# Kernel tuning notes

Hardware: AMD Instinct MI355X
Metric: run time of the kernel (lower is better)

The kernel has to match this reference:

```python
import jax, jax.numpy as jnp
import numpy as np

DIM = 1024
WIN = 7
HEADS = 16
HEAD_DIM = DIM // HEADS
NT = WIN * WIN  # tokens per window = 49


def _relative_position_index():
    coords = np.stack(np.meshgrid(np.arange(WIN), np.arange(WIN), indexing='ij'))  # [2,W,W]
    cf = coords.reshape(2, -1)  # [2, NT]
    rel = cf[:, :, None] - cf[:, None, :]  # [2, NT, NT]
    rel = rel.transpose(1, 2, 0).copy()
    rel[:, :, 0] += WIN - 1
    rel[:, :, 1] += WIN - 1
    rel[:, :, 0] *= 2 * WIN - 1
    return jnp.asarray(rel.sum(-1), dtype=jnp.int32)  # [NT, NT]

REL_IDX = _relative_position_index()


def setup_inputs() -> dict:
    key = jax.random.key(0)
    ks = jax.random.split(key, 7)
    bsz_windows = 2048
    num_windows = 64
    x = jax.random.normal(ks[0], (bsz_windows, NT, DIM), dtype=jnp.float32)
    attn_mask = jax.random.normal(ks[1], (num_windows, NT, NT), dtype=jnp.float32)
    s = 0.02
    qkv_w = jax.random.normal(ks[2], (3 * DIM, DIM), dtype=jnp.float32) * s
    qkv_b = jnp.zeros((3 * DIM,), dtype=jnp.float32)
    proj_w = jax.random.normal(ks[3], (DIM, DIM), dtype=jnp.float32) * s
    proj_b = jnp.zeros((DIM,), dtype=jnp.float32)
    bias_table = jax.random.normal(ks[4], ((2 * WIN - 1) ** 2, HEADS), dtype=jnp.float32) * s
    return {"x": x, "attn_mask": attn_mask, "qkv_w": qkv_w, "qkv_b": qkv_b,
            "proj_w": proj_w, "proj_b": proj_b, "bias_table": bias_table}


def reference(x, attn_mask, qkv_w, qkv_b, proj_w, proj_b, bias_table):
    bw, nt, c = x.shape
    scale = HEAD_DIM ** -0.5
    qkv = x @ qkv_w.T + qkv_b  # [bw, nt, 3*dim]
    qkv = qkv.reshape(bw, nt, 3, HEADS, HEAD_DIM).transpose(2, 0, 3, 1, 4)
    q, k, v = qkv[0], qkv[1], qkv[2]  # each [bw, h, nt, hd]
    attn = jnp.einsum('bhqd,bhkd->bhqk', q * scale, k)  # [bw, h, nt, nt]
    rel_bias = bias_table[REL_IDX.reshape(-1)].reshape(nt, nt, HEADS).transpose(2, 0, 1)
    attn = attn + rel_bias[None]
    nw = attn_mask.shape[0]
    attn = attn.reshape(bw // nw, nw, HEADS, nt, nt) + attn_mask[None, :, None]
    attn = attn.reshape(bw, HEADS, nt, nt)
    attn = jax.nn.softmax(attn, axis=-1)
    out = jnp.einsum('bhqk,bhkd->bhqd', attn, v)
    out = out.transpose(0, 2, 1, 3).reshape(bw, nt, c)
    return out @ proj_w.T + proj_b
```

## Files before the change

kernel.cpp:

```cpp
#include <hip/hip_runtime.h>
#include <hip/hip_bf16.h>
#include <cstdint>
#include <cstddef>

#define HEADS 16
#define HD 64
#define NT 49
#define NTOK 3136
#define MROWS 100352
#define KDIM 1024

typedef __attribute__((ext_vector_type(4))) float f32x4;
typedef __attribute__((ext_vector_type(8))) short bf16x8;
typedef __attribute__((ext_vector_type(4))) unsigned short u16x4;

__device__ __forceinline__ unsigned short f2b(float f) {
  __hip_bfloat16 h = __float2bfloat16(f);
  return *reinterpret_cast<unsigned short*>(&h);
}
__device__ __forceinline__ float b2f(unsigned short u) {
  union { unsigned int i; float f; } c; c.i = ((unsigned int)u) << 16; return c.f;
}

__device__ __forceinline__ void gload16(const unsigned short* g, void* l) {
  __builtin_amdgcn_global_load_lds(
      (const __attribute__((address_space(1))) void*)g,
      (__attribute__((address_space(3))) void*)l, 16, 0, 0);
}

__device__ __forceinline__ void bar() {
  asm volatile("" ::: "memory");
  __builtin_amdgcn_s_barrier();
  asm volatile("" ::: "memory");
}

__global__ void cvt_f32_bf16(const float* __restrict__ s,
                             unsigned short* __restrict__ d, long n4) {
  long stride = (long)gridDim.x * blockDim.x;
  for (long i = blockIdx.x * (long)blockDim.x + threadIdx.x; i < n4; i += stride) {
    f32x4 v = reinterpret_cast<const f32x4*>(s)[i];
    u16x4 o;
    o.x = f2b(v.x); o.y = f2b(v.y); o.z = f2b(v.z); o.w = f2b(v.w);
    reinterpret_cast<u16x4*>(d)[i] = o;
  }
}

__global__ void build_bm(const float* __restrict__ mask,
                         const float* __restrict__ bias_table,
                         float* __restrict__ bm) {
  const int wm = blockIdx.x >> 4, h = blockIdx.x & 15;
  const float* mrow = mask + (size_t)wm * (NT * NT);
  float* dst = bm + ((size_t)wm * HEADS + h) * (NT * 64);
  for (int idx = threadIdx.x; idx < NT * 64; idx += 256) {
    const int a = idx >> 6, b = idx & 63;
    float v = -1e30f;
    if (b < NT) {
      const int ia = a / 7, ja = a - ia * 7;
      const int ib = b / 7, jb = b - ib * 7;
      v = mrow[a * NT + b] +
          bias_table[((ia - ib + 6) * 13 + (ja - jb + 6)) * HEADS + h];
    }
    dst[idx] = v;
  }
}

template<int EPI>
__global__ __launch_bounds__(512, 2)
void gemm_bt(const unsigned short* __restrict__ A,
             const unsigned short* __restrict__ B,
             const float* __restrict__ bias,
             void* __restrict__ Cout,
             const int nTilesN) {
  __shared__ __align__(16) unsigned short lds[2 * 2 * 256 * 64];

  const int nwg = gridDim.x;
  const int bid = blockIdx.x;
  const int cpx = nwg >> 3;
  const int swz = (bid & 7) * cpx + (bid >> 3);
  const int mt = swz / nTilesN;
  const int nt = swz - mt * nTilesN;
  const long mBase = (long)mt * 256;
  const int nBase = nt * 256;

  const int tid = threadIdx.x;
  const int lane = tid & 63;
  const int wid = tid >> 6;
  const int wr = wid >> 2;
  const int wc = wid & 3;
  const int lr = lane & 15;
  const int kg = lane >> 4;

  const int rbase = tid >> 3;
  const int c8 = (((tid & 7) ^ (rbase & 7)) << 3);
  const unsigned short* aSrc = A + (size_t)(mBase + rbase) * KDIM + c8;
  const unsigned short* bSrc = B + (size_t)(nBase + rbase) * KDIM + c8;
  char* ldsB = (char*)lds;

  f32x4 acc[8][4] = {};

  const int aRow = (wr * 128 + lr) * 64;
  const int bRow = (wc * 64 + lr) * 64;
  const int fOff0 = ((0 * 4 + kg) ^ (lr & 7)) << 3;
  const int fOff1 = ((1 * 4 + kg) ^ (lr & 7)) << 3;

#define STAGE(buf, kt) do {                                         \
    char* dA = ldsB + (buf) * 65536 + tid * 16;                     \
    const unsigned short* sA = aSrc + (kt) * 64;                    \
    const unsigned short* sB = bSrc + (kt) * 64;                    \
    _Pragma("unroll")                                               \
    for (int j = 0; j < 4; ++j)                                     \
      gload16(sA + (size_t)j * 64 * KDIM, dA + j * 8192);           \
    _Pragma("unroll")                                               \
    for (int j = 0; j < 4; ++j)                                     \
      gload16(sB + (size_t)j * 64 * KDIM, dA + 32768 + j * 8192);   \
  } while (0)

  STAGE(0, 0);
  STAGE(1, 1);
  asm volatile("s_waitcnt vmcnt(8)" ::: "memory");
  __builtin_amdgcn_sched_barrier(0);
  bar();

  for (int kt = 0; kt < KDIM / 64; ++kt) {
    const int cb = kt & 1;
    const unsigned short* As = lds + cb * 32768;
    const unsigned short* Bs = As + 16384;

    bf16x8 a0[4], a1[4], a2[4], a3[4], b0[4], b1[4];

#pragma unroll
    for (int j = 0; j < 4; ++j)
      a0[j] = *reinterpret_cast<const bf16x8*>(As + aRow + j * 1024 + fOff0);
#pragma unroll
    for (int n = 0; n < 4; ++n)
      b0[n] = *reinterpret_cast<const bf16x8*>(Bs + bRow + n * 1024 + fOff0);

    __builtin_amdgcn_s_setprio(1);
#pragma unroll
    for (int j = 0; j < 4; ++j)
      a1[j] = *reinterpret_cast<const bf16x8*>(As + aRow + (4 + j) * 1024 + fOff0);
#pragma unroll
    for (int j = 0; j < 4; ++j)
#pragma unroll
      for (int n = 0; n < 4; ++n)
        acc[j][n] = __builtin_amdgcn_mfma_f32_16x16x32_bf16(
            a0[j], b0[n], acc[j][n], 0, 0, 0);
    __builtin_amdgcn_s_setprio(0);
    bar();

    __builtin_amdgcn_s_setprio(1);
#pragma unroll
    for (int j = 0; j < 4; ++j)
      a2[j] = *reinterpret_cast<const bf16x8*>(As + aRow + j * 1024 + fOff1);
#pragma unroll
    for (int n = 0; n < 4; ++n)
      b1[n] = *reinterpret_cast<const bf16x8*>(Bs + bRow + n * 1024 + fOff1);
#pragma unroll
    for (int j = 0; j < 4; ++j)
#pragma unroll
      for (int n = 0; n < 4; ++n)
        acc[4 + j][n] = __builtin_amdgcn_mfma_f32_16x16x32_bf16(
            a1[j], b0[n], acc[4 + j][n], 0, 0, 0);
    __builtin_amdgcn_s_setprio(0);
    bar();

    __builtin_amdgcn_s_setprio(1);
#pragma unroll
    for (int j = 0; j < 4; ++j)
      a3[j] = *reinterpret_cast<const bf16x8*>(As + aRow + (4 + j) * 1024 + fOff1);
#pragma unroll
    for (int j = 0; j < 4; ++j)
#pragma unroll
      for (int n = 0; n < 4; ++n)
        acc[j][n] = __builtin_amdgcn_mfma_f32_16x16x32_bf16(
            a2[j], b1[n], acc[j][n], 0, 0, 0);
    __builtin_amdgcn_s_setprio(0);
    bar();

    __builtin_amdgcn_s_setprio(1);
#pragma unroll
    for (int j = 0; j < 4; ++j)
#pragma unroll
      for (int n = 0; n < 4; ++n)
        acc[4 + j][n] = __builtin_amdgcn_mfma_f32_16x16x32_bf16(
            a3[j], b1[n], acc[4 + j][n], 0, 0, 0);
    __builtin_amdgcn_s_setprio(0);
    bar();

    if (kt < KDIM / 64 - 2) {
      STAGE(cb, kt + 2);
      asm volatile("s_waitcnt vmcnt(8)" ::: "memory");
      __builtin_amdgcn_sched_barrier(0);
      bar();
    } else if (kt == KDIM / 64 - 2) {
      asm volatile("s_waitcnt vmcnt(0)" ::: "memory");
      __builtin_amdgcn_sched_barrier(0);
      bar();
    }
  }
#undef STAGE

  if (EPI == 0) {
    unsigned short* qkvbuf = (unsigned short*)Cout;
#pragma unroll
    for (int m = 0; m < 8; ++m) {
      const int row0 = wr * 128 + m * 16 + kg * 4;
#pragma unroll
      for (int n = 0; n < 4; ++n) {
        const int col = nBase + wc * 64 + n * 16 + lr;
        const int which = col >> 10;
        const int head = (col >> 6) & 15;
        const int d = col & 63;
        const float bv = bias[col];
#pragma unroll
        for (int r = 0; r < 4; ++r) {
          const int gm = (int)mBase + row0 + r;
          const int w = gm / NT;
          const int t = gm - w * NT;
          float v = acc[m][n][r] + bv;
          if (which == 0) v *= 0.125f;
          qkvbuf[(((size_t)w * 3 + which) * HEADS + head) * NTOK + t * HD + d] =
              f2b(v);
        }
      }
    }
  } else {
    float* out = (float*)Cout;
#pragma unroll
    for (int m = 0; m < 8; ++m) {
      const int row0 = wr * 128 + m * 16 + kg * 4;
#pragma unroll
      for (int n = 0; n < 4; ++n) {
        const int col = nBase + wc * 64 + n * 16 + lr;
        const float bv = bias[col];
#pragma unroll
        for (int r = 0; r < 4; ++r) {
          const int gm = (int)mBase + row0 + r;
          out[(size_t)gm * KDIM + col] = acc[m][n][r] + bv;
        }
      }
    }
  }
}

#define PSTR 72
#define VTSTR 72

__global__ __launch_bounds__(256, 8)
void attn_mfma(const unsigned short* __restrict__ qkv,
               const float* __restrict__ bm,
               unsigned short* __restrict__ aout) {
  const int blk = blockIdx.x;
  const int w = blk >> 4;
  const int h = blk & 15;
  const int tid = threadIdx.x;
  const int lane = tid & 63;
  const int wv = tid >> 6;
  const int lr = lane & 15;
  const int kg = lane >> 4;

  __shared__ __align__(16) unsigned short Plds[64 * PSTR];
  __shared__ __align__(16) unsigned short VldsT[64 * VTSTR];

  const unsigned short* qp = qkv + (((size_t)w * 3 + 0) * HEADS + h) * NTOK;
  const unsigned short* kp = qp + (size_t)HEADS * NTOK;
  const unsigned short* vp = qp + (size_t)2 * HEADS * NTOK;
  const float* bmrow = bm + (((size_t)(w & 63) * HEADS + h) * (NT * 64));

  const int a0 = wv * 16 + kg * 4;
  f32x4 acc[4];
#pragma unroll
  for (int r = 0; r < 4; ++r) {
    const int a = a0 + r;
    const int ar = (a > 48) ? 48 : a;
#pragma unroll
    for (int n = 0; n < 4; ++n)
      acc[n][r] = bmrow[ar * 64 + n * 16 + lr];
  }

#pragma unroll
  for (int i = 0; i < 4; ++i) {
    const int idx = i * 256 + tid;
    if (idx < 784) {
      const int t = idx >> 4, c4 = (idx & 15) * 4;
      u16x4 vv = *reinterpret_cast<const u16x4*>(vp + t * HD + c4);
      const int ts = t >> 3, t7 = t & 7;
#pragma unroll
      for (int ii = 0; ii < 4; ++ii) {
        const int d = c4 + ii;
        VldsT[d * VTSTR + (((ts ^ (d & 7)) << 3) + t7)] =
            ((const unsigned short*)&vv)[ii];
      }
    }
  }
#pragma unroll
  for (int i = 0; i < 4; ++i) {
    const int idx = i * 256 + tid;
    if (idx < 960) {
      const int d = idx / 15, t = 49 + idx - d * 15;
      VldsT[d * VTSTR + ((((t >> 3) ^ (d & 7)) << 3) + (t & 7))] = 0;
    }
  }
  __syncthreads();

  int qrow = wv * 16 + lr; if (qrow > 48) qrow = 48;
#pragma unroll
  for (int ks = 0; ks < 2; ++ks) {
    bf16x8 af = *reinterpret_cast<const bf16x8*>(qp + qrow * HD + ks * 32 + kg * 8);
#pragma unroll
    for (int n = 0; n < 4; ++n) {
      int row = n * 16 + lr; if (row > 48) row = 48;
      bf16x8 bfr = *reinterpret_cast<const bf16x8*>(kp + row * HD + ks * 32 + kg * 8);
      acc[n] = __builtin_amdgcn_mfma_f32_16x16x32_bf16(af, bfr, acc[n], 0, 0, 0);
    }
  }

#pragma unroll
  for (int r = 0; r < 4; ++r) {
    float mx = fmaxf(fmaxf(acc[0][r], acc[1][r]),
                     fmaxf(acc[2][r], acc[3][r]));
    mx = fmaxf(mx, __shfl_xor(mx, 1));
    mx = fmaxf(mx, __shfl_xor(mx, 2));
    mx = fmaxf(mx, __shfl_xor(mx, 4));
    mx = fmaxf(mx, __shfl_xor(mx, 8));
    float s = 0.f;
#pragma unroll
    for (int n = 0; n < 4; ++n) {
      const float e = __expf(acc[n][r] - mx);
      acc[n][r] = e;
      s += e;
    }
    s += __shfl_xor(s, 1);
    s += __shfl_xor(s, 2);
    s += __shfl_xor(s, 4);
    s += __shfl_xor(s, 8);
    const float si = 1.0f / s;
#pragma unroll
    for (int n = 0; n < 4; ++n) acc[n][r] *= si;
  }

#pragma unroll
  for (int n = 0; n < 4; ++n)
#pragma unroll
    for (int r = 0; r < 4; ++r)
      Plds[(a0 + r) * PSTR + n * 16 + lr] = f2b(acc[n][r]);

  f32x4 acc2[4] = {};
  const int prow = wv * 16 + lr;
#pragma unroll
  for (int ks = 0; ks < 2; ++ks) {
    bf16x8 pf = *reinterpret_cast<const bf16x8*>(
        &Plds[prow * PSTR + ks * 32 + kg * 8]);
#pragma unroll
    for (int n = 0; n < 4; ++n) {
      const int d = n * 16 + lr;
      bf16x8 vf = *reinterpret_cast<const bf16x8*>(
          &VldsT[d * VTSTR + ((((ks * 4 + kg) ^ (d & 7)) << 3))]);
      acc2[n] = __builtin_amdgcn_mfma_f32_16x16x32_bf16(pf, vf, acc2[n], 0, 0, 0);
    }
  }

#pragma unroll
  for (int r = 0; r < 4; ++r) {
    const int a = a0 + r;
    if (a >= NT) continue;
#pragma unroll
    for (int n = 0; n < 4; ++n) {
      const int d = n * 16 + lr;
      aout[((size_t)(w * NT + a)) * KDIM + h * HD + d] = f2b(acc2[n][r]);
    }
  }
}

extern "C" void kernel_launch(void* const* d_in, const int* in_sizes, int n_in,
                              void* d_out, int out_size, void* d_ws, size_t ws_size,
                              hipStream_t stream) {
  const float* x          = (const float*)d_in[0];
  const float* attn_mask  = (const float*)d_in[1];
  const float* qkv_w      = (const float*)d_in[2];
  const float* qkv_b      = (const float*)d_in[3];
  const float* proj_w     = (const float*)d_in[4];
  const float* proj_b     = (const float*)d_in[5];
  const float* bias_table = (const float*)d_in[6];
  float* out = (float*)d_out;

  char* ws = (char*)d_ws;
  const size_t xbf_bytes = (size_t)MROWS * KDIM * 2;
  const size_t qkv_bytes = (size_t)2048 * 3 * HEADS * NTOK * 2;
  unsigned short* xbf      = (unsigned short*)ws;
  unsigned short* qkvw_bf  = (unsigned short*)(ws + xbf_bytes);
  unsigned short* projw_bf = qkvw_bf + 3072 * 1024;
  unsigned short* qkvbuf   = (unsigned short*)(ws + xbf_bytes + 8388608);
  float* bm                = (float*)(ws + xbf_bytes + 8388608 + qkv_bytes);
  unsigned short* aout     = xbf;

  build_bm<<<64 * HEADS, 256, 0, stream>>>(attn_mask, bias_table, bm);

  cvt_f32_bf16<<<8192, 256, 0, stream>>>(x, xbf, (long)MROWS * KDIM / 4);
  cvt_f32_bf16<<<3072, 256, 0, stream>>>(qkv_w, qkvw_bf, (long)3072 * 1024 / 4);
  cvt_f32_bf16<<<1024, 256, 0, stream>>>(proj_w, projw_bf, (long)1024 * 1024 / 4);

  gemm_bt<0><<<392 * 12, 512, 0, stream>>>(xbf, qkvw_bf, qkv_b, (void*)qkvbuf, 12);

  attn_mfma<<<2048 * HEADS, 256, 0, stream>>>(qkvbuf, bm, aout);

  gemm_bt<1><<<392 * 4, 512, 0, stream>>>(aout, projw_bf, proj_b, (void*)out, 4);
}
```

Baseline: 1.375 ms.

## Shrink GEMM tiles to 256x128 with K-step 32 for higher occupancy

Reworks the bf16 GEMM from a 256x256 output tile with K-step 64 to a 256x128 tile with K-step 32. The warp layout becomes 4x2 waves with 4x4 MFMA accumulators each, which cuts LDS use and register pressure so the launch bounds can ask for 4 blocks per CU. The LDS swizzle and staging are redone to match, and both GEMM grids double. The trade is less data reuse per tile, so more global and LDS traffic per FLOP, and twice as many barriers per unit of K.

```diff
diff --git a/kernel.cpp b/kernel.cpp
--- a/kernel.cpp
+++ b/kernel.cpp
@@ -65,13 +65,13 @@
 }
 
 template<int EPI>
-__global__ __launch_bounds__(512, 2)
+__global__ __launch_bounds__(512, 4)
 void gemm_bt(const unsigned short* __restrict__ A,
              const unsigned short* __restrict__ B,
              const float* __restrict__ bias,
              void* __restrict__ Cout,
              const int nTilesN) {
-  __shared__ __align__(16) unsigned short lds[2 * 2 * 256 * 64];
+  __shared__ __align__(16) unsigned short lds[2 * 12288];
 
   const int nwg = gridDim.x;
   const int bid = blockIdx.x;
@@ -80,119 +80,79 @@
   const int mt = swz / nTilesN;
   const int nt = swz - mt * nTilesN;
   const long mBase = (long)mt * 256;
-  const int nBase = nt * 256;
+  const int nBase = nt * 128;
 
   const int tid = threadIdx.x;
   const int lane = tid & 63;
   const int wid = tid >> 6;
-  const int wr = wid >> 2;
-  const int wc = wid & 3;
+  const int wr = wid >> 1;
+  const int wc = wid & 1;
   const int lr = lane & 15;
   const int kg = lane >> 4;
 
-  const int rbase = tid >> 3;
-  const int c8 = (((tid & 7) ^ (rbase & 7)) << 3);
-  const unsigned short* aSrc = A + (size_t)(mBase + rbase) * KDIM + c8;
-  const unsigned short* bSrc = B + (size_t)(nBase + rbase) * KDIM + c8;
+  const int srow = tid >> 2;
+  const int c8 = (((tid & 3) ^ ((tid >> 3) & 3)) << 3);
+  const unsigned short* aSrc0 = A + (size_t)(mBase + srow) * KDIM + c8;
+  const unsigned short* aSrc1 = aSrc0 + (size_t)128 * KDIM;
+  const unsigned short* bSrc  = B + (size_t)(nBase + srow) * KDIM + c8;
   char* ldsB = (char*)lds;
 
-  f32x4 acc[8][4] = {};
-
-  const int aRow = (wr * 128 + lr) * 64;
-  const int bRow = (wc * 64 + lr) * 64;
-  const int fOff0 = ((0 * 4 + kg) ^ (lr & 7)) << 3;
-  const int fOff1 = ((1 * 4 + kg) ^ (lr & 7)) << 3;
-
-#define STAGE(buf, kt) do {                                         \
-    char* dA = ldsB + (buf) * 65536 + tid * 16;                     \
-    const unsigned short* sA = aSrc + (kt) * 64;                    \
-    const unsigned short* sB = bSrc + (kt) * 64;                    \
-    _Pragma("unroll")                                               \
-    for (int j = 0; j < 4; ++j)                                     \
-      gload16(sA + (size_t)j * 64 * KDIM, dA + j * 8192);           \
-    _Pragma("unroll")                                               \
-    for (int j = 0; j < 4; ++j)                                     \
-      gload16(sB + (size_t)j * 64 * KDIM, dA + 32768 + j * 8192);   \
+  f32x4 acc[4][4] = {};
+
+  int aOff[4], bOff[4];
+#pragma unroll
+  for (int m = 0; m < 4; ++m) {
+    const int row = wr * 64 + m * 16 + lr;
+    aOff[m] = row * 32 + ((kg ^ ((row >> 1) & 3)) << 3);
+  }
+#pragma unroll
+  for (int n = 0; n < 4; ++n) {
+    const int row = wc * 64 + n * 16 + lr;
+    bOff[n] = row * 32 + ((kg ^ ((row >> 1) & 3)) << 3);
+  }
+
+#define STAGE(buf, kt) do {                               \
+    char* dst = ldsB + (buf) * 24576 + tid * 16;          \
+    gload16(aSrc0 + (kt) * 32, dst);                      \
+    gload16(aSrc1 + (kt) * 32, dst + 8192);               \
+    gload16(bSrc  + (kt) * 32, dst + 16384);              \
   } while (0)
 
   STAGE(0, 0);
   STAGE(1, 1);
-  asm volatile("s_waitcnt vmcnt(8)" ::: "memory");
+  asm volatile("s_waitcnt vmcnt(3)" ::: "memory");
   __builtin_amdgcn_sched_barrier(0);
   bar();
 
-  for (int kt = 0; kt < KDIM / 64; ++kt) {
+  for (int kt = 0; kt < KDIM / 32; ++kt) {
     const int cb = kt & 1;
-    const unsigned short* As = lds + cb * 32768;
-    const unsigned short* Bs = As + 16384;
-
-    bf16x8 a0[4], a1[4], a2[4], a3[4], b0[4], b1[4];
-
-#pragma unroll
-    for (int j = 0; j < 4; ++j)
-      a0[j] = *reinterpret_cast<const bf16x8*>(As + aRow + j * 1024 + fOff0);
+    const unsigned short* As = lds + cb * 12288;
+    const unsigned short* Bs = As + 8192;
+
+    bf16x8 af[4], bfv[4];
+#pragma unroll
+    for (int m = 0; m < 4; ++m)
+      af[m] = *reinterpret_cast<const bf16x8*>(As + aOff[m]);
 #pragma unroll
     for (int n = 0; n < 4; ++n)
-      b0[n] = *reinterpret_cast<const bf16x8*>(Bs + bRow + n * 1024 + fOff0);
+      bfv[n] = *reinterpret_cast<const bf16x8*>(Bs + bOff[n]);
 
     __builtin_amdgcn_s_setprio(1);
 #pragma unroll
-    for (int j = 0; j < 4; ++j)
-      a1[j] = *reinterpret_cast<const bf16x8*>(As + aRow + (4 + j) * 1024 + fOff0);
-#pragma unroll
-    for (int j = 0; j < 4; ++j)
+    for (int m = 0; m < 4; ++m)
 #pragma unroll
       for (int n = 0; n < 4; ++n)
-        acc[j][n] = __builtin_amdgcn_mfma_f32_16x16x32_bf16(
-            a0[j], b0[n], acc[j][n], 0, 0, 0);
+        acc[m][n] = __builtin_amdgcn_mfma_f32_16x16x32_bf16(
+            af[m], bfv[n], acc[m][n], 0, 0, 0);
     __builtin_amdgcn_s_setprio(0);
     bar();
 
-    __builtin_amdgcn_s_setprio(1);
-#pragma unroll
-    for (int j = 0; j < 4; ++j)
-      a2[j] = *reinterpret_cast<const bf16x8*>(As + aRow + j * 1024 + fOff1);
-#pragma unroll
-    for (int n = 0; n < 4; ++n)
-      b1[n] = *reinterpret_cast<const bf16x8*>(Bs + bRow + n * 1024 + fOff1);
-#pragma unroll
-    for (int j = 0; j < 4; ++j)
-#pragma unroll
-      for (int n = 0; n < 4; ++n)
-        acc[4 + j][n] = __builtin_amdgcn_mfma_f32_16x16x32_bf16(
-            a1[j], b0[n], acc[4 + j][n], 0, 0, 0);
-    __builtin_amdgcn_s_setprio(0);
-    bar();
-
-    __builtin_amdgcn_s_setprio(1);
-#pragma unroll
-    for (int j = 0; j < 4; ++j)
-      a3[j] = *reinterpret_cast<const bf16x8*>(As + aRow + (4 + j) * 1024 + fOff1);
-#pragma unroll
-    for (int j = 0; j < 4; ++j)
-#pragma unroll
-      for (int n = 0; n < 4; ++n)
-        acc[j][n] = __builtin_amdgcn_mfma_f32_16x16x32_bf16(
-            a2[j], b1[n], acc[j][n], 0, 0, 0);
-    __builtin_amdgcn_s_setprio(0);
-    bar();
-
-    __builtin_amdgcn_s_setprio(1);
-#pragma unroll
-    for (int j = 0; j < 4; ++j)
-#pragma unroll
-      for (int n = 0; n < 4; ++n)
-        acc[4 + j][n] = __builtin_amdgcn_mfma_f32_16x16x32_bf16(
-            a3[j], b1[n], acc[4 + j][n], 0, 0, 0);
-    __builtin_amdgcn_s_setprio(0);
-    bar();
-
-    if (kt < KDIM / 64 - 2) {
+    if (kt < KDIM / 32 - 2) {
       STAGE(cb, kt + 2);
-      asm volatile("s_waitcnt vmcnt(8)" ::: "memory");
+      asm volatile("s_waitcnt vmcnt(3)" ::: "memory");
       __builtin_amdgcn_sched_barrier(0);
       bar();
-    } else if (kt == KDIM / 64 - 2) {
+    } else if (kt == KDIM / 32 - 2) {
       asm volatile("s_waitcnt vmcnt(0)" ::: "memory");
       __builtin_amdgcn_sched_barrier(0);
       bar();
@@ -203,8 +163,8 @@
   if (EPI == 0) {
     unsigned short* qkvbuf = (unsigned short*)Cout;
 #pragma unroll
-    for (int m = 0; m < 8; ++m) {
-      const int row0 = wr * 128 + m * 16 + kg * 4;
+    for (int m = 0; m < 4; ++m) {
+      const int row0 = wr * 64 + m * 16 + kg * 4;
 #pragma unroll
       for (int n = 0; n < 4; ++n) {
         const int col = nBase + wc * 64 + n * 16 + lr;
@@ -227,8 +187,8 @@
   } else {
     float* out = (float*)Cout;
 #pragma unroll
-    for (int m = 0; m < 8; ++m) {
-      const int row0 = wr * 128 + m * 16 + kg * 4;
+    for (int m = 0; m < 4; ++m) {
+      const int row0 = wr * 64 + m * 16 + kg * 4;
 #pragma unroll
       for (int n = 0; n < 4; ++n) {
         const int col = nBase + wc * 64 + n * 16 + lr;
@@ -400,9 +360,9 @@
   cvt_f32_bf16<<<3072, 256, 0, stream>>>(qkv_w, qkvw_bf, (long)3072 * 1024 / 4);
   cvt_f32_bf16<<<1024, 256, 0, stream>>>(proj_w, projw_bf, (long)1024 * 1024 / 4);
 
-  gemm_bt<0><<<392 * 12, 512, 0, stream>>>(xbf, qkvw_bf, qkv_b, (void*)qkvbuf, 12);
+  gemm_bt<0><<<392 * 24, 512, 0, stream>>>(xbf, qkvw_bf, qkv_b, (void*)qkvbuf, 24);
 
   attn_mfma<<<2048 * HEADS, 256, 0, stream>>>(qkvbuf, bm, aout);
 
-  gemm_bt<1><<<392 * 4, 512, 0, stream>>>(aout, projw_bf, proj_b, (void*)out, 4);
-}
+  gemm_bt<1><<<392 * 8, 512, 0, stream>>>(aout, projw_bf, proj_b, (void*)out, 8);
+}
```

Result: no change. 1.360 ms (-1.1%).
